# Kernel optimization log

Hardware: AMD Instinct MI355X
Metric: run time of the kernel (lower is better)

Reference implementation:

```python
import jax, jax.numpy as jnp
import numpy as np

N_HEAD = 16
CHUNK = 128  # block size for the causal linear-attention scan


def _phi(x):
    return jax.nn.elu(x) + 1.0


def setup_inputs() -> dict:
    key = jax.random.key(0)
    k1, k2, k3 = jax.random.split(key, 3)
    B, T, E = 4, 2048, 1024
    x = jax.random.normal(k1, (B, T, E), dtype=jnp.float32)
    w_attn = jax.random.normal(k2, (3 * E, E), dtype=jnp.float32) * 0.02
    w_proj = jax.random.normal(k3, (E, E), dtype=jnp.float32) * 0.02
    return {"x": x, "w_attn": w_attn, "w_proj": w_proj}


def _causal_linear_attn(qp, kp, v):
    # qp, kp, v: [B, H, T, D]; phi already applied to qp, kp
    B, H, T, D = qp.shape
    NC = T // CHUNK

    def to_chunks(a):  # -> [NC, B, H, CHUNK, D]
        return a.reshape(B, H, NC, CHUNK, D).transpose(2, 0, 1, 3, 4)

    qc, kc, vc = to_chunks(qp), to_chunks(kp), to_chunks(v)
    mask = jnp.tril(jnp.ones((CHUNK, CHUNK), dtype=bool))

    def step(carry, blk):
        S, z = carry  # S: [B,H,D,D] = sum_{prev} k v^T ; z: [B,H,D] = sum_{prev} k
        q_c, k_c, v_c = blk  # [B,H,CHUNK,D]
        scores = jnp.einsum('bhcd,bhkd->bhck', q_c, k_c)
        scores = jnp.where(mask, scores, 0.0)
        num = (jnp.einsum('bhck,bhke->bhce', scores, v_c)
               + jnp.einsum('bhcd,bhde->bhce', q_c, S))
        den = scores.sum(-1) + jnp.einsum('bhcd,bhd->bhc', q_c, z)
        S = S + jnp.einsum('bhkd,bhke->bhde', k_c, v_c)
        z = z + k_c.sum(axis=2)
        return (S, z), (num, den)

    S0 = jnp.zeros((B, H, D, D), dtype=qp.dtype)
    z0 = jnp.zeros((B, H, D), dtype=qp.dtype)
    _, (num, den) = jax.lax.scan(step, (S0, z0), (qc, kc, vc))
    y = num / (den[..., None] + 1e-6)  # [NC,B,H,CHUNK,D]
    y = y.transpose(1, 2, 0, 3, 4).reshape(B, H, T, D)
    return y


def reference(x, w_attn, w_proj):
    B, T, E = x.shape
    H = N_HEAD
    D = E // H
    qkv = x @ w_attn.T  # [B,T,3E]
    q, k, v = jnp.split(qkv, 3, axis=2)

    def heads(a):  # [B,T,E] -> [B,H,T,D]
        return a.reshape(B, T, H, D).transpose(0, 2, 1, 3)

    y = _causal_linear_attn(_phi(heads(q)), _phi(heads(k)), heads(v))
    y = y.transpose(0, 2, 1, 3).reshape(B, T, E)
    return y @ w_proj.T
```

## Files before the change

### kernel.cpp

```cpp
#include <hip/hip_runtime.h>
#include <math.h>

#define B_ 4
#define T_ 2048
#define E_ 1024
#define H_ 16
#define D_ 64
#define CHUNK_ 128
#define NC_ 16
#define BH_ (B_ * H_)
#define M_ (B_ * T_)

typedef __attribute__((ext_vector_type(8))) short bf16x8;
typedef __attribute__((ext_vector_type(4))) float f32x4;

__device__ __forceinline__ ushort rnbf(float f) {
  unsigned u = __float_as_uint(f);
  unsigned r = (u + 0x7FFFu + ((u >> 16) & 1u)) >> 16;
  return (ushort)r;
}

__device__ __forceinline__ float bf2f(short s) {
  return __uint_as_float(((unsigned)(ushort)s) << 16);
}

__device__ __forceinline__ void gload_lds16(const void* g, void* l) {
  __builtin_amdgcn_global_load_lds(
      (const __attribute__((address_space(1))) unsigned int*)g,
      (__attribute__((address_space(3))) unsigned int*)l, 16, 0, 0);
}

#define VMW(N) do { asm volatile("s_waitcnt vmcnt(" #N ")" ::: "memory"); \
                    __builtin_amdgcn_sched_barrier(0); } while (0)
#define BARR() do { __builtin_amdgcn_s_barrier(); \
                    __builtin_amdgcn_sched_barrier(0); } while (0)
#define LGK0() do { asm volatile("s_waitcnt lgkmcnt(0)" ::: "memory"); \
                    __builtin_amdgcn_sched_barrier(0); } while (0)

#define N4X_ (M_ * E_ / 4)
#define N4A_ (3 * E_ * E_ / 4)
#define N4P_ (E_ * E_ / 4)
__global__ __launch_bounds__(256) void k_cvt3(
    const float* __restrict__ x, const float* __restrict__ wa,
    const float* __restrict__ wp, ushort* __restrict__ xb,
    ushort* __restrict__ wab, ushort* __restrict__ wpb) {
  int i = blockIdx.x * 256 + threadIdx.x;
  const float* src;
  ushort* dst;
  int off;
  if (i < N4X_) { src = x; dst = xb; off = i; }
  else if (i < N4X_ + N4A_) { src = wa; dst = wab; off = i - N4X_; }
  else { src = wp; dst = wpb; off = i - (N4X_ + N4A_); }
  float4 v = ((const float4*)src)[off];
  ushort4 o;
  o.x = rnbf(v.x); o.y = rnbf(v.y); o.z = rnbf(v.z); o.w = rnbf(v.w);
  ((ushort4*)dst)[off] = o;
}

#define STG(sl_, tt_) { \
  gload_lds16(Asrc + (tt_) * 32, &lds[(sl_) * 4096 + tid * 8]); \
  gload_lds16(Bsrc0 + (tt_) * 32, &lds[12288 + (sl_) * 8192 + tid * 8]); \
  gload_lds16(Bsrc1 + (tt_) * 32, &lds[12288 + (sl_) * 8192 + 4096 + tid * 8]); }

#define LDFRAGS(sl_) \
  const ushort* pa = &lds[(sl_) * 4096 + aOff]; \
  a0 = *(const bf16x8*)pa;          a1 = *(const bf16x8*)(pa + 512); \
  a2 = *(const bf16x8*)(pa + 1024); a3 = *(const bf16x8*)(pa + 1536); \
  const ushort* pb = &lds[12288 + (sl_) * 8192 + bOff]; \
  b0 = *(const bf16x8*)pb;          b1 = *(const bf16x8*)(pb + 512); \
  b2 = *(const bf16x8*)(pb + 1024); b3 = *(const bf16x8*)(pb + 1536);

#define MM(i, j, A_, B_) \
  acc[i][j] = __builtin_amdgcn_mfma_f32_16x16x32_bf16(A_, B_, acc[i][j], 0, 0, 0)
#define MFMA16() do { __builtin_amdgcn_s_setprio(1); \
  MM(0,0,a0,b0); MM(0,1,a0,b1); MM(0,2,a0,b2); MM(0,3,a0,b3); \
  MM(1,0,a1,b0); MM(1,1,a1,b1); MM(1,2,a1,b2); MM(1,3,a1,b3); \
  MM(2,0,a2,b0); MM(2,1,a2,b1); MM(2,2,a2,b2); MM(2,3,a2,b3); \
  MM(3,0,a3,b0); MM(3,1,a3,b1); MM(3,2,a3,b2); MM(3,3,a3,b3); \
  __builtin_amdgcn_s_setprio(0); } while (0)

__device__ __forceinline__ void pipe_gemm(const ushort* __restrict__ Ag,
                                          const ushort* __restrict__ Bg,
                                          ushort* lds, f32x4 acc[4][4]) {
  const int tid = threadIdx.x;
  const int l = tid & 63, wv = tid >> 6;
  const int wm = wv >> 2, wn = wv & 3;
  const int c16 = l & 15, g4 = l >> 4;
  const int gch = (tid & 3) ^ ((tid >> 3) & 3);
  const ushort* Asrc = Ag + (size_t)(tid >> 2) * 1024 + gch * 8;
  const ushort* Bsrc0 = Bg + (size_t)(tid >> 2) * 1024 + gch * 8;
  const ushort* Bsrc1 = Bsrc0 + (size_t)128 * 1024;
  const int xq = (c16 >> 1) & 3;
  const int aOff = (wm * 64 + c16) * 32 + ((g4 ^ xq) << 3);
  const int bOff = (wn * 64 + c16) * 32 + ((g4 ^ xq) << 3);

  STG(0, 0);
  STG(1, 1);
  int sl = 0;
#pragma unroll 3
  for (int t = 0; t < 30; ++t) {
    const int slN = sl ? sl - 1 : 2;
    VMW(3); BARR();
    bf16x8 a0, a1, a2, a3, b0, b1, b2, b3;
    LDFRAGS(sl);
    STG(slN, t + 2);
    MFMA16();
    sl = (sl == 2) ? 0 : sl + 1;
  }
  {
    VMW(3); BARR();
    bf16x8 a0, a1, a2, a3, b0, b1, b2, b3;
    LDFRAGS(0);
    MFMA16();
  }
  {
    VMW(0); BARR();
    bf16x8 a0, a1, a2, a3, b0, b1, b2, b3;
    LDFRAGS(1);
    MFMA16();
  }
}

__global__ __launch_bounds__(512, 4) void k_qkv2(
    const ushort* __restrict__ xb, const ushort* __restrict__ wab,
    ushort* __restrict__ qg, ushort* __restrict__ kg,
    ushort* __restrict__ ktg, ushort* __restrict__ vtg,
    float* __restrict__ zp) {
  extern __shared__ ushort lds[];
  const int b = blockIdx.x;
  const int xcd = b & 7, idx = b >> 3;
  const int bm = xcd * 8 + (idx & 7);
  const int bn = idx >> 3;
  const int tid = threadIdx.x;
  const int wv = tid >> 6, l = tid & 63;
  const int wm = wv >> 2, wn = wv & 3;
  const int c16 = l & 15, g4 = l >> 4;

  f32x4 acc[4][4] = {};
  pipe_gemm(xb + (size_t)bm * 128 * 1024, wab + (size_t)bn * 256 * 1024, lds, acc);

  BARR();
  const int colbase = bn * 256 + wn * 64;
  const int which = colbase >> 10;
  const int h = (colbase & 1023) >> 6;
  const int rowbase = bm * 128 + wm * 64;
  const int bidx = rowbase >> 11;
  const int tbase = rowbase & 2047;
  const size_t bh = (size_t)(bidx * 16 + h);
  ushort* wlds = &lds[wv * 4096];
  float zpart[4] = {0.f, 0.f, 0.f, 0.f};
#pragma unroll
  for (int mf = 0; mf < 4; ++mf) {
#pragma unroll
    for (int nf = 0; nf < 4; ++nf) {
      float o[4];
#pragma unroll
      for (int j = 0; j < 4; ++j) {
        float u = acc[mf][nf][j];
        o[j] = (which < 2) ? ((u > 0.f) ? u + 1.f : expf(u)) : u;
      }
      const int d = nf * 16 + c16;
      if (which == 1) zpart[nf] += o[0] + o[1] + o[2] + o[3];
      if (which <= 1) {
        ushort* dst = (which == 0) ? qg : kg;
        const size_t rb = (bh * 2048 + tbase + mf * 16 + g4 * 4) * 64 + d;
#pragma unroll
        for (int j = 0; j < 4; ++j) dst[rb + (size_t)j * 64] = rnbf(o[j]);
      }
      if (which >= 1) {
        const int tb = (mf * 4 + g4) ^ ((d & 3) << 1);
        ushort4 pk;
        pk.x = rnbf(o[0]); pk.y = rnbf(o[1]); pk.z = rnbf(o[2]); pk.w = rnbf(o[3]);
        *(ushort4*)&wlds[d * 64 + tb * 4] = pk;
      }
    }
  }
  if (which == 1) {
    const int cc = tbase >> 7;
#pragma unroll
    for (int nf = 0; nf < 4; ++nf) {
      float zz = zpart[nf];
      zz += __shfl_xor(zz, 16);
      zz += __shfl_xor(zz, 32);
      if (l < 16) zp[((bh * NC_ + cc) * 2 + wm) * 64 + nf * 16 + l] = zz;
    }
  }
  if (which >= 1) {
    asm volatile("s_waitcnt lgkmcnt(0)" ::: "memory");
    __builtin_amdgcn_sched_barrier(0);
    ushort* tg = (which == 1) ? ktg : vtg;
#pragma unroll
    for (int it = 0; it < 8; ++it) {
      const int d = it * 8 + (l >> 3);
      const int t0 = (l & 7) * 8;
      const int blk = ((l & 7) * 2) ^ ((d & 3) << 1);
      bf16x8 vv_ = *(const bf16x8*)&wlds[d * 64 + blk * 4];
      *(bf16x8*)&tg[(bh * 64 + d) * 2048 + tbase + t0] = vv_;
    }
  }
}

__global__ __launch_bounds__(512, 4) void k_proj2(
    const ushort* __restrict__ yb, const ushort* __restrict__ wpb,
    float* __restrict__ out) {
  extern __shared__ ushort lds[];
  const int b = blockIdx.x;
  const int xcd = b & 7, idx = b >> 3;
  const int bm = xcd * 8 + (idx & 7);
  const int bn = idx >> 3;
  const int tid = threadIdx.x;
  const int wv = tid >> 6, l = tid & 63;
  const int wm = wv >> 2, wn = wv & 3;
  const int c16 = l & 15, g4 = l >> 4;

  f32x4 acc[4][4] = {};
  pipe_gemm(yb + (size_t)bm * 128 * 1024, wpb + (size_t)bn * 256 * 1024, lds, acc);

  const int rowbase = bm * 128 + wm * 64 + g4 * 4;
  const int colbase = bn * 256 + wn * 64 + c16;
#pragma unroll
  for (int mf = 0; mf < 4; ++mf)
#pragma unroll
    for (int nf = 0; nf < 4; ++nf) {
      const size_t base = (size_t)(rowbase + mf * 16) * 1024 + colbase + nf * 16;
#pragma unroll
      for (int j = 0; j < 4; ++j)
        out[base + (size_t)j * 1024] = acc[mf][nf][j];
    }
}

__global__ __launch_bounds__(256) void k_stats(const ushort* __restrict__ ktg,
                                               const ushort* __restrict__ vtg,
                                               float* __restrict__ Sc) {
  __shared__ __align__(16) ushort kT_s[64 * 128], vT_s[64 * 128];
  const int blk = blockIdx.x;
  const int bh = blk >> 4, c = blk & 15;
  const int tid = threadIdx.x;
  const int w = tid >> 6, l = tid & 63;
  const ushort* ktb = ktg + (size_t)bh * D_ * T_ + c * CHUNK_;
  const ushort* vtb = vtg + (size_t)bh * D_ * T_ + c * CHUNK_;
#pragma unroll
  for (int s2 = 0; s2 < 4; ++s2) {
    const int seg = w * 4 + s2;
    const int row = seg * 4 + (l >> 4);
    const int sb = ((l & 15) ^ (row & 7)) * 8;
    gload_lds16(ktb + (size_t)row * T_ + sb, &kT_s[seg * 512]);
    gload_lds16(vtb + (size_t)row * T_ + sb, &vT_s[seg * 512]);
  }
  __syncthreads();
  const int wr = w >> 1, wc = w & 1;
  f32x4 acc[2][2] = {};
#pragma unroll
  for (int kt = 0; kt < 4; ++kt) {
    const int g = kt * 32 + (l >> 4) * 8;
    bf16x8 av[2], bk[2];
#pragma unroll
    for (int rt = 0; rt < 2; ++rt) {
      const int e = wr * 32 + rt * 16 + (l & 15);
      av[rt] = *(const bf16x8*)&vT_s[e * 128 + (g ^ ((e & 7) << 3))];
    }
#pragma unroll
    for (int ct = 0; ct < 2; ++ct) {
      const int d = wc * 32 + ct * 16 + (l & 15);
      bk[ct] = *(const bf16x8*)&kT_s[d * 128 + (g ^ ((d & 7) << 3))];
    }
#pragma unroll
    for (int rt = 0; rt < 2; ++rt)
#pragma unroll
      for (int ct = 0; ct < 2; ++ct)
        acc[rt][ct] = __builtin_amdgcn_mfma_f32_16x16x32_bf16(av[rt], bk[ct],
                                                              acc[rt][ct], 0, 0, 0);
  }
  float* So = Sc + (size_t)blk * 4096;
#pragma unroll
  for (int rt = 0; rt < 2; ++rt)
#pragma unroll
    for (int ct = 0; ct < 2; ++ct)
#pragma unroll
      for (int jj = 0; jj < 4; ++jj)
        So[(wr * 32 + rt * 16 + (l >> 4) * 4 + jj) * 64 + wc * 32 + ct * 16 + (l & 15)] =
            acc[rt][ct][jj];
}

__global__ __launch_bounds__(256) void k_prefix2(const float* __restrict__ Sc,
                                                 ushort* __restrict__ STb,
                                                 const float* __restrict__ zp,
                                                 float* __restrict__ zout) {
  const int b = blockIdx.x;
  const int tid = threadIdx.x;
  if (b < 256) {
    const int bh = b >> 2, qt = b & 3;
    const float4* Sb = (const float4*)(Sc + (size_t)bh * NC_ * 4096) + qt * 256 + tid;
    ushort4* Ob = (ushort4*)(STb + (size_t)bh * NC_ * 4096) + qt * 256 + tid;
    float4 v[16];
#pragma unroll
    for (int c = 0; c < NC_; ++c) v[c] = Sb[c * 1024];
    float4 acc = make_float4(0.f, 0.f, 0.f, 0.f);
#pragma unroll
    for (int c = 0; c < NC_; ++c) {
      ushort4 o;
      o.x = rnbf(acc.x); o.y = rnbf(acc.y); o.z = rnbf(acc.z); o.w = rnbf(acc.w);
      Ob[c * 1024] = o;
      acc.x += v[c].x; acc.y += v[c].y; acc.z += v[c].z; acc.w += v[c].w;
    }
  } else {
    const int bh = b - 256;
    if (tid < 16) {
      const float4* zpb = (const float4*)(zp + (size_t)bh * NC_ * 128);
      float4* zob = (float4*)(zout + (size_t)bh * NC_ * 64);
      float4 t0[16], t1[16];
#pragma unroll
      for (int c = 0; c < NC_; ++c) {
        t0[c] = zpb[c * 32 + tid];
        t1[c] = zpb[c * 32 + 16 + tid];
      }
      float4 za = make_float4(0.f, 0.f, 0.f, 0.f);
#pragma unroll
      for (int c = 0; c < NC_; ++c) {
        zob[c * 16 + tid] = za;
        za.x += t0[c].x + t1[c].x; za.y += t0[c].y + t1[c].y;
        za.z += t0[c].z + t1[c].z; za.w += t0[c].w + t1[c].w;
      }
    }
  }
}

__global__ __launch_bounds__(512, 4) void k_out(
    const ushort* __restrict__ qg, const ushort* __restrict__ kg,
    const ushort* __restrict__ vtg, const ushort* __restrict__ STb,
    const float* __restrict__ zg, ushort* __restrict__ yb) {
  __shared__ __align__(16) ushort k_s[128 * 64];
  __shared__ __align__(16) ushort vT_s[64 * 128];
  __shared__ __align__(16) ushort ST_s[64 * 64];
  __shared__ __align__(16) ushort P_s[128 * 128];
  __shared__ float z_s[64];
  __shared__ float dinter_s[128];
  const int blk = blockIdx.x;
  const int bh = blk >> 4, c = blk & 15;
  const int tid = threadIdx.x;
  const int w = tid >> 6, l = tid & 63;

  const ushort* kbase = kg + ((size_t)bh * T_ + c * CHUNK_) * D_;
  const ushort* vbase = vtg + (size_t)bh * D_ * T_ + c * CHUNK_;
  const ushort* sbase = STb + ((size_t)bh * NC_ + c) * 4096;
  {
    int seg = w, row = seg * 8 + (l >> 3);
    gload_lds16(kbase + (size_t)row * 64 + ((l & 7) ^ (row & 7)) * 8, &k_s[seg * 512]);
    seg = w + 8; row = seg * 8 + (l >> 3);
    gload_lds16(kbase + (size_t)row * 64 + ((l & 7) ^ (row & 7)) * 8, &k_s[seg * 512]);
  }
  {
    int seg = w, row = seg * 4 + (l >> 4);
    gload_lds16(vbase + (size_t)row * T_ + ((l & 15) ^ (row & 7)) * 8, &vT_s[seg * 512]);
    seg = w + 8; row = seg * 4 + (l >> 4);
    gload_lds16(vbase + (size_t)row * T_ + ((l & 15) ^ (row & 7)) * 8, &vT_s[seg * 512]);
  }
  {
    const int seg = w, row = seg * 8 + (l >> 3);
    gload_lds16(sbase + (size_t)row * 64 + ((l & 7) ^ (row & 7)) * 8, &ST_s[seg * 512]);
  }
  if (tid < 64) z_s[tid] = zg[((size_t)bh * NC_ + c) * 64 + tid];
  const int arow = w * 16 + (l & 15);
  const ushort* qrow = qg + ((size_t)bh * T_ + c * CHUNK_ + arow) * D_ + (l >> 4) * 8;
  bf16x8 qf0 = *(const bf16x8*)(qrow);
  bf16x8 qf1 = *(const bf16x8*)(qrow + 32);
  __syncthreads();

  const int crow0 = w * 16 + (l >> 4) * 4;
  float rsum[4] = {0.f, 0.f, 0.f, 0.f};
  for (int jt = 0; jt <= w; ++jt) {
    const int j = jt * 16 + (l & 15);
    const int sw = (j & 7) << 3, g = (l >> 4) * 8;
    bf16x8 b0 = *(const bf16x8*)&k_s[j * 64 + (g ^ sw)];
    bf16x8 b1 = *(const bf16x8*)&k_s[j * 64 + ((g + 32) ^ sw)];
    f32x4 s4 = {0.f, 0.f, 0.f, 0.f};
    s4 = __builtin_amdgcn_mfma_f32_16x16x32_bf16(qf0, b0, s4, 0, 0, 0);
    s4 = __builtin_amdgcn_mfma_f32_16x16x32_bf16(qf1, b1, s4, 0, 0, 0);
#pragma unroll
    for (int jj = 0; jj < 4; ++jj) {
      const int i = crow0 + jj;
      float s = (j <= i) ? s4[jj] : 0.f;
      rsum[jj] += s;
      P_s[i * 128 + (j ^ ((i & 7) << 3))] = rnbf(s);
    }
  }
  if (!(w & 1)) {
    const int j = (w + 1) * 16 + (l & 15);
#pragma unroll
    for (int jj = 0; jj < 4; ++jj) {
      const int i = crow0 + jj;
      P_s[i * 128 + (j ^ ((i & 7) << 3))] = 0;
    }
  }
  float di = 0.f;
#pragma unroll
  for (int jj = 0; jj < 8; ++jj) {
    di = fmaf(bf2f(qf0[jj]), z_s[(l >> 4) * 8 + jj], di);
    di = fmaf(bf2f(qf1[jj]), z_s[32 + (l >> 4) * 8 + jj], di);
  }
  di += __shfl_xor(di, 16);
  di += __shfl_xor(di, 32);
  if (l < 16) dinter_s[w * 16 + l] = di;
#pragma unroll
  for (int jj = 0; jj < 4; ++jj) {
    float r = rsum[jj];
    r += __shfl_xor(r, 1); r += __shfl_xor(r, 2);
    r += __shfl_xor(r, 4); r += __shfl_xor(r, 8);
    rsum[jj] = r;
  }
  LGK0();

  f32x4 acc2[4] = {};
#pragma unroll
  for (int et = 0; et < 4; ++et) {
    const int e = et * 16 + (l & 15);
    const int sw = (e & 7) << 3, g = (l >> 4) * 8;
    bf16x8 s0 = *(const bf16x8*)&ST_s[e * 64 + (g ^ sw)];
    bf16x8 s1 = *(const bf16x8*)&ST_s[e * 64 + ((g + 32) ^ sw)];
    acc2[et] = __builtin_amdgcn_mfma_f32_16x16x32_bf16(qf0, s0, acc2[et], 0, 0, 0);
    acc2[et] = __builtin_amdgcn_mfma_f32_16x16x32_bf16(qf1, s1, acc2[et], 0, 0, 0);
  }
  const int prow = w * 16 + (l & 15);
  const int psw = (prow & 7) << 3;
  for (int jkt = 0; jkt <= (w >> 1); ++jkt) {
    bf16x8 pa = *(const bf16x8*)&P_s[prow * 128 + ((jkt * 32 + (l >> 4) * 8) ^ psw)];
#pragma unroll
    for (int et = 0; et < 4; ++et) {
      const int e = et * 16 + (l & 15);
      bf16x8 bv = *(const bf16x8*)&vT_s[e * 128 +
                                        ((jkt * 32 + (l >> 4) * 8) ^ ((e & 7) << 3))];
      acc2[et] = __builtin_amdgcn_mfma_f32_16x16x32_bf16(pa, bv, acc2[et], 0, 0, 0);
    }
  }
  float inv[4];
#pragma unroll
  for (int jj = 0; jj < 4; ++jj)
    inv[jj] = 1.0f / (rsum[jj] + dinter_s[crow0 + jj] + 1e-6f);
  const int b = bh >> 4, h = bh & 15;
#pragma unroll
  for (int et = 0; et < 4; ++et) {
    const int d = et * 16 + (l & 15);
#pragma unroll
    for (int jj = 0; jj < 4; ++jj) {
      const int t = c * CHUNK_ + crow0 + jj;
      yb[((size_t)(b * T_ + t) * H_ + h) * D_ + d] = rnbf(acc2[et][jj] * inv[jj]);
    }
  }
}

extern "C" void kernel_launch(void* const* d_in, const int* in_sizes, int n_in,
                              void* d_out, int out_size, void* d_ws, size_t ws_size,
                              hipStream_t stream) {
  const float* x = (const float*)d_in[0];
  const float* w_attn = (const float*)d_in[1];
  const float* w_proj = (const float*)d_in[2];
  float* out = (float*)d_out;

  ushort* xb = (ushort*)d_ws;
  ushort* wab = xb + (size_t)M_ * E_;
  ushort* wpb = wab + (size_t)3 * E_ * E_;
  ushort* qb = wpb + (size_t)E_ * E_;
  ushort* kbm = qb + (size_t)M_ * E_;
  ushort* kT = kbm + (size_t)M_ * E_;
  ushort* vT = kT + (size_t)M_ * E_;
  ushort* yb = vT + (size_t)M_ * E_;
  ushort* STb = yb + (size_t)M_ * E_;
  float* Schunk = (float*)(STb + (size_t)BH_ * NC_ * 4096);
  float* zpart = Schunk + (size_t)BH_ * NC_ * 4096;
  float* zout = zpart + (size_t)BH_ * NC_ * 2 * 64;

  k_cvt3<<<12288, 256, 0, stream>>>(x, w_attn, w_proj, xb, wab, wpb);

  hipFuncSetAttribute((const void*)k_qkv2,
                      hipFuncAttributeMaxDynamicSharedMemorySize, 73728);
  hipFuncSetAttribute((const void*)k_proj2,
                      hipFuncAttributeMaxDynamicSharedMemorySize, 73728);

  k_qkv2<<<768, 512, 73728, stream>>>(xb, wab, qb, kbm, kT, vT, zpart);
  k_stats<<<1024, 256, 0, stream>>>(kT, vT, Schunk);
  k_prefix2<<<320, 256, 0, stream>>>(Schunk, STb, zpart, zout);
  k_out<<<1024, 512, 0, stream>>>(qb, kbm, vT, STb, zout, yb);
  k_proj2<<<256, 512, 73728, stream>>>(yb, wpb, out);
}
```

Before: 128.6 us.

## Retile output projection GEMM to 128x128 tiles with 256-thread blocks and triple-buffered LDS

Replaces the output projection kernel's 128x256 tile on 512 threads with a 128x128 tile on 256 threads (4 waves of 64x64), doubling the grid to 512 blocks. It adds a custom 3-slot LDS pipeline with swizzled direct global-to-LDS loads, prefetching two K-steps ahead. The aim is better CU occupancy and load balance for the 8192x1024x1024 GEMM, at the cost of less operand reuse per block and more global traffic for the A tile.

```diff
diff --git a/kernel.cpp b/kernel.cpp
--- a/kernel.cpp
+++ b/kernel.cpp
@@ -200,7 +200,24 @@
   }
 }
 
-__global__ __launch_bounds__(512, 4) void k_proj2(
+#define APB(sl_) ((sl_) * 4096)
+#define BPB(sl_) (12288 + (sl_) * 4096)
+
+#define STGP(sl_, tt_) { \
+  gload_lds16(Asrc + (tt_) * 32,         &lds[APB(sl_) + tid * 8]); \
+  gload_lds16(Asrc + (tt_) * 32 + 65536, &lds[APB(sl_) + 2048 + tid * 8]); \
+  gload_lds16(Bsrc + (tt_) * 32,         &lds[BPB(sl_) + tid * 8]); \
+  gload_lds16(Bsrc + (tt_) * 32 + 65536, &lds[BPB(sl_) + 2048 + tid * 8]); }
+
+#define LDFRAGSP(sl_) \
+  const ushort* pa = &lds[APB(sl_) + aOff]; \
+  a0 = *(const bf16x8*)pa;          a1 = *(const bf16x8*)(pa + 512); \
+  a2 = *(const bf16x8*)(pa + 1024); a3 = *(const bf16x8*)(pa + 1536); \
+  const ushort* pb = &lds[BPB(sl_) + bOff]; \
+  b0 = *(const bf16x8*)pb;          b1 = *(const bf16x8*)(pb + 512); \
+  b2 = *(const bf16x8*)(pb + 1024); b3 = *(const bf16x8*)(pb + 1536);
+
+__global__ __launch_bounds__(256, 2) void k_proj3(
     const ushort* __restrict__ yb, const ushort* __restrict__ wpb,
     float* __restrict__ out) {
   extern __shared__ ushort lds[];
@@ -210,14 +227,48 @@
   const int bn = idx >> 3;
   const int tid = threadIdx.x;
   const int wv = tid >> 6, l = tid & 63;
-  const int wm = wv >> 2, wn = wv & 3;
+  const int wm = wv >> 1, wn = wv & 1;
   const int c16 = l & 15, g4 = l >> 4;
 
+  const ushort* Ag = yb + (size_t)bm * 128 * 1024;
+  const ushort* Bg = wpb + (size_t)bn * 128 * 1024;
+  const int gch = (tid & 3) ^ ((tid >> 3) & 3);
+  const ushort* Asrc = Ag + (size_t)(tid >> 2) * 1024 + gch * 8;
+  const ushort* Bsrc = Bg + (size_t)(tid >> 2) * 1024 + gch * 8;
+  const int xq = (c16 >> 1) & 3;
+  const int aOff = (wm * 64 + c16) * 32 + ((g4 ^ xq) << 3);
+  const int bOff = (wn * 64 + c16) * 32 + ((g4 ^ xq) << 3);
+
   f32x4 acc[4][4] = {};
-  pipe_gemm(yb + (size_t)bm * 128 * 1024, wpb + (size_t)bn * 256 * 1024, lds, acc);
+
+  STGP(0, 0);
+  STGP(1, 1);
+  int sl = 0;
+#pragma unroll 3
+  for (int t = 0; t < 30; ++t) {
+    const int slN = sl ? sl - 1 : 2;
+    VMW(4); BARR();
+    bf16x8 a0, a1, a2, a3, b0, b1, b2, b3;
+    LDFRAGSP(sl);
+    STGP(slN, t + 2);
+    MFMA16();
+    sl = (sl == 2) ? 0 : sl + 1;
+  }
+  {
+    VMW(4); BARR();
+    bf16x8 a0, a1, a2, a3, b0, b1, b2, b3;
+    LDFRAGSP(0);
+    MFMA16();
+  }
+  {
+    VMW(0); BARR();
+    bf16x8 a0, a1, a2, a3, b0, b1, b2, b3;
+    LDFRAGSP(1);
+    MFMA16();
+  }
 
   const int rowbase = bm * 128 + wm * 64 + g4 * 4;
-  const int colbase = bn * 256 + wn * 64 + c16;
+  const int colbase = bn * 128 + wn * 64 + c16;
 #pragma unroll
   for (int mf = 0; mf < 4; ++mf)
 #pragma unroll
@@ -473,12 +524,12 @@
 
   hipFuncSetAttribute((const void*)k_qkv2,
                       hipFuncAttributeMaxDynamicSharedMemorySize, 73728);
-  hipFuncSetAttribute((const void*)k_proj2,
-                      hipFuncAttributeMaxDynamicSharedMemorySize, 73728);
+  hipFuncSetAttribute((const void*)k_proj3,
+                      hipFuncAttributeMaxDynamicSharedMemorySize, 49152);
 
   k_qkv2<<<768, 512, 73728, stream>>>(xb, wab, qb, kbm, kT, vT, zpart);
   k_stats<<<1024, 256, 0, stream>>>(kT, vT, Schunk);
   k_prefix2<<<320, 256, 0, stream>>>(Schunk, STb, zpart, zout);
   k_out<<<1024, 512, 0, stream>>>(qb, kbm, vT, STb, zout, yb);
-  k_proj2<<<256, 512, 73728, stream>>>(yb, wpb, out);
-}
+  k_proj3<<<512, 256, 49152, stream>>>(yb, wpb, out);
+}
```

New measurement: 127.6 us. Within noise of the previous version (-0.7%).
